# Performance work log

Measured on AMD Instinct MI355X. Metric: run time of the kernel, lower is better.

## Reference

```python
import jax, jax.numpy as jnp
import numpy as np

NHEAD = 8  # nn.MultiheadAttention default in TransformerDecoderLayerOptimal
LN_EPS = 1e-5


def layer_norm(x, g, b):
    m = x.mean(-1, keepdims=True)
    v = ((x - m) ** 2).mean(-1, keepdims=True)
    return (x - m) * jax.lax.rsqrt(v + LN_EPS) * g + b


def setup_inputs() -> dict:
    key = jax.random.key(0)
    ks = jax.random.split(key, 16)
    B, S, F0, D, L, C, DF = 32, 1024, 2048, 768, 100, 1000, 10
    sc = 0.02
    return {
        "x": jax.random.normal(ks[0], (B, S, F0), jnp.float32),
        "y": jax.random.normal(ks[1], (L, D), jnp.float32),
        "embed_W": jax.random.normal(ks[2], (D, F0), jnp.float32) * sc,
        "embed_b": jnp.zeros((D,), jnp.float32),
        "Wq": jax.random.normal(ks[3], (D, D), jnp.float32) * sc,
        "Wk": jax.random.normal(ks[4], (D, D), jnp.float32) * sc,
        "Wv": jax.random.normal(ks[5], (D, D), jnp.float32) * sc,
        "bq": jnp.zeros((D,), jnp.float32),
        "bk": jnp.zeros((D,), jnp.float32),
        "bv": jnp.zeros((D,), jnp.float32),
        "Wo": jax.random.normal(ks[6], (D, D), jnp.float32) * sc,
        "bo": jnp.zeros((D,), jnp.float32),
        "ln1_g": jnp.ones((D,), jnp.float32), "ln1_b": jnp.zeros((D,), jnp.float32),
        "ln2_g": jnp.ones((D,), jnp.float32), "ln2_b": jnp.zeros((D,), jnp.float32),
        "ln3_g": jnp.ones((D,), jnp.float32), "ln3_b": jnp.zeros((D,), jnp.float32),
        "ffn_W1": jax.random.normal(ks[7], (D, D), jnp.float32) * sc,  # dim_feedforward = d_model
        "ffn_b1": jnp.zeros((D,), jnp.float32),
        "ffn_W2": jax.random.normal(ks[8], (D, D), jnp.float32) * sc,
        "ffn_b2": jnp.zeros((D,), jnp.float32),
        "dup_pool": jax.random.normal(ks[9], (L, 2 * D, DF), jnp.float32) * sc,
        "dup_bias": jnp.zeros((C,), jnp.float32),
    }


def reference(x, y, embed_W, embed_b, Wq, Wk, Wv, bq, bk, bv, Wo, bo,
              ln1_g, ln1_b, ln2_g, ln2_b, ln3_g, ln3_b,
              ffn_W1, ffn_b1, ffn_W2, ffn_b2, dup_pool, dup_bias):
    B = x.shape[0]
    L, D = y.shape
    H, hd = NHEAD, D // NHEAD
    num_classes = dup_bias.shape[0]

    # embed_standart + relu : (B,S,F0) -> (B,S,D)
    mem = jax.nn.relu(jnp.einsum('bsf,df->bsd', x, embed_W) + embed_b)

    # tgt = query_embed repeated over batch (batch-first here)
    tgt0 = jnp.broadcast_to(y[None], (B, L, D))

    # TransformerDecoderLayerOptimal (eval mode: dropout = identity)
    t = layer_norm(tgt0 + tgt0, ln1_g, ln1_b)  # tgt + dropout1(tgt)

    # cross multi-head attention
    q = (jnp.einsum('bld,ed->ble', t, Wq) + bq).reshape(B, L, H, hd)
    k = (jnp.einsum('bsd,ed->bse', mem, Wk) + bk).reshape(B, -1, H, hd)
    v = (jnp.einsum('bsd,ed->bse', mem, Wv) + bv).reshape(B, -1, H, hd)
    scores = jnp.einsum('blhe,bshe->bhls', q, k) / np.float32(np.sqrt(hd))
    attn = jax.nn.softmax(scores, axis=-1)           # (B,H,L,S)
    ao = jnp.einsum('bhls,bshe->blhe', attn, v).reshape(B, L, D)
    ao = jnp.einsum('bld,ed->ble', ao, Wo) + bo
    t = layer_norm(t + ao, ln2_g, ln2_b)

    # FFN
    f = jnp.einsum('bld,ed->ble',
                   jax.nn.relu(jnp.einsum('bld,ed->ble', t, ffn_W1) + ffn_b1),
                   ffn_W2) + ffn_b2
    h = layer_norm(t + f, ln3_g, ln3_b)              # (B,L,D)

    # concat label embedding after h, then GroupFC (per-label grouped matmul)
    hcat = jnp.concatenate([h, tgt0], axis=-1)       # (B,L,2D)
    out_extrap = jnp.einsum('bld,ldf->blf', hcat, dup_pool)  # (B,L,DF)
    logits = out_extrap.reshape(B, -1)[:, :num_classes] + dup_bias

    a_score = attn.mean(axis=1)                      # MHA averages heads: (B,L,S)
    return logits, a_score
```

## Files before the change

### kernel.cpp

```cpp
#include <hip/hip_runtime.h>

typedef unsigned short u16;
typedef __bf16 bf16x8 __attribute__((ext_vector_type(8)));
typedef short s16x8 __attribute__((ext_vector_type(8)));
typedef u16 u16x4 __attribute__((ext_vector_type(4)));
typedef float f32x4 __attribute__((ext_vector_type(4)));

__device__ __forceinline__ float b2f(u16 u) {
  union { unsigned u32; float f; } x; x.u32 = ((unsigned)u) << 16; return x.f;
}
__device__ __forceinline__ u16 f2b(float f) {
  union { float f; unsigned u; } x; x.f = f;
  unsigned r = x.u + 0x7fffu + ((x.u >> 16) & 1u);
  return (u16)(r >> 16);
}

template <int F32>
__device__ __forceinline__ s16x8 load8(const void* __restrict__ p, size_t idx) {
  if (F32) {
    const float* f = (const float*)p + idx;
    f32x4 a = *(const f32x4*)f;
    f32x4 b = *(const f32x4*)(f + 4);
    s16x8 r;
    r[0] = (short)f2b(a[0]); r[1] = (short)f2b(a[1]);
    r[2] = (short)f2b(a[2]); r[3] = (short)f2b(a[3]);
    r[4] = (short)f2b(b[0]); r[5] = (short)f2b(b[1]);
    r[6] = (short)f2b(b[2]); r[7] = (short)f2b(b[3]);
    return r;
  } else {
    return *(const s16x8*)((const u16*)p + idx);
  }
}

template <int RELU, int AF32, int BF32, int TRANSC = 0>
__global__ __launch_bounds__(256) void gemm_bt_kernel(
    const void* __restrict__ A, const void* __restrict__ Bt,
    const float* __restrict__ bias, u16* __restrict__ C,
    int M, int N, int K) {
  __shared__ u16 As[128][32];
  __shared__ u16 Bs[128][32];
  const int tid = threadIdx.x;
  const int lane = tid & 63;
  const int wave = tid >> 6;
  const int wm = wave >> 1, wn = wave & 1;
  const int lr = tid >> 2;
  const int lk = (tid & 3) << 3;
  const int tn = blockIdx.x, tm = blockIdx.y;
  const size_t abase = (size_t)tm * 128 * K;
  const size_t bbase = (size_t)tn * 128 * K;
  const int fr = lane & 15;
  const int fk = (lane >> 4) << 3;
  f32x4 acc[4][4] = {};

  for (int k0 = 0; k0 < K; k0 += 32) {
    *(s16x8*)&As[lr][lk]      = load8<AF32>(A, abase + (size_t)lr * K + k0 + lk);
    *(s16x8*)&As[lr + 64][lk] = load8<AF32>(A, abase + (size_t)(lr + 64) * K + k0 + lk);
    *(s16x8*)&Bs[lr][lk]      = load8<BF32>(Bt, bbase + (size_t)lr * K + k0 + lk);
    *(s16x8*)&Bs[lr + 64][lk] = load8<BF32>(Bt, bbase + (size_t)(lr + 64) * K + k0 + lk);
    __syncthreads();
    bf16x8 af[4], bfv[4];
#pragma unroll
    for (int i = 0; i < 4; ++i)
      af[i] = __builtin_bit_cast(bf16x8, *(const s16x8*)&As[wm * 64 + i * 16 + fr][fk]);
#pragma unroll
    for (int j = 0; j < 4; ++j)
      bfv[j] = __builtin_bit_cast(bf16x8, *(const s16x8*)&Bs[wn * 64 + j * 16 + fr][fk]);
#pragma unroll
    for (int i = 0; i < 4; ++i)
#pragma unroll
      for (int j = 0; j < 4; ++j)
        acc[i][j] = __builtin_amdgcn_mfma_f32_16x16x32_bf16(af[i], bfv[j], acc[i][j], 0, 0, 0);
    __syncthreads();
  }

  const int row0 = tm * 128 + wm * 64 + ((lane >> 4) << 2);
  const int col0 = tn * 128 + wn * 64 + fr;
  if (TRANSC) {
#pragma unroll
    for (int j = 0; j < 4; ++j) {
      const int col = col0 + j * 16;
      const float bv = bias[col];
#pragma unroll
      for (int i = 0; i < 4; ++i) {
        const int row = row0 + i * 16;
        u16x4 pk;
#pragma unroll
        for (int r = 0; r < 4; ++r) {
          float v = acc[i][j][r] + bv;
          if (RELU) v = fmaxf(v, 0.f);
          pk[r] = f2b(v);
        }
        size_t idx = ((size_t)(row >> 10) * N + col) * 1024 + (row & 1023);
        *(u16x4*)&C[idx] = pk;
      }
    }
  } else {
#pragma unroll
    for (int j = 0; j < 4; ++j) {
      const int col = col0 + j * 16;
      const float bv = bias[col];
#pragma unroll
      for (int i = 0; i < 4; ++i) {
#pragma unroll
        for (int r = 0; r < 4; ++r) {
          float v = acc[i][j][r] + bv;
          if (RELU) v = fmaxf(v, 0.f);
          C[(size_t)(row0 + i * 16 + r) * N + col] = f2b(v);
        }
      }
    }
  }
}

__device__ __forceinline__ void block_stats(float s, float s2, float* red, int tid,
                                            float& S, float& S2) {
#pragma unroll
  for (int o = 32; o > 0; o >>= 1) { s += __shfl_xor(s, o); s2 += __shfl_xor(s2, o); }
  if ((tid & 63) == 0) { red[tid >> 6] = s; red[4 + (tid >> 6)] = s2; }
  __syncthreads();
  S = red[0] + red[1] + red[2] + red[3];
  S2 = red[4] + red[5] + red[6] + red[7];
}

__global__ __launch_bounds__(256) void t_kernel(const float* __restrict__ y,
                                                const float* __restrict__ g,
                                                const float* __restrict__ bb,
                                                float* __restrict__ t) {
  const int l = blockIdx.x, tid = threadIdx.x;
  __shared__ float red[8];
  float xv[3], s = 0.f, s2 = 0.f;
#pragma unroll
  for (int i = 0; i < 3; ++i) {
    int e = tid + i * 256;
    float v = 2.f * y[(size_t)l * 768 + e];
    xv[i] = v; s += v; s2 += v * v;
  }
  float S, S2;
  block_stats(s, s2, red, tid, S, S2);
  float mean = S * (1.f / 768.f);
  float var = S2 * (1.f / 768.f) - mean * mean;
  float inv = rsqrtf(var + 1e-5f);
#pragma unroll
  for (int i = 0; i < 3; ++i) {
    int e = tid + i * 256;
    t[(size_t)l * 768 + e] = (xv[i] - mean) * inv * g[e] + bb[e];
  }
}

__global__ __launch_bounds__(256) void q_kernel(const float* __restrict__ t,
                                                const float* __restrict__ Wq,
                                                const float* __restrict__ bq,
                                                float* __restrict__ q) {
  const int l = blockIdx.x, tid = threadIdx.x;
  __shared__ __align__(16) float ts[768];
  for (int i = tid; i < 768; i += 256) ts[i] = t[(size_t)l * 768 + i];
  __syncthreads();
  for (int e = tid; e < 768; e += 256) {
    const float* wr = Wq + (size_t)e * 768;
    float acc = bq[e];
    for (int j = 0; j < 768; j += 4) {
      f32x4 wv = *(const f32x4*)&wr[j];
      f32x4 tv = *(const f32x4*)&ts[j];
      acc += wv[0] * tv[0] + wv[1] * tv[1] + wv[2] * tv[2] + wv[3] * tv[3];
    }
    q[(size_t)l * 768 + e] = acc;
  }
}

__global__ __launch_bounds__(256) void c2_kernel(const float* __restrict__ y,
                                                 const float* __restrict__ pool,
                                                 const float* __restrict__ dbias,
                                                 float* __restrict__ c2) {
  const int l = blockIdx.x, tid = threadIdx.x, lane = tid & 63, w = tid >> 6;
  for (int j = w; j < 10; j += 4) {
    float acc = 0.f;
    for (int d = lane; d < 768; d += 64)
      acc += y[(size_t)l * 768 + d] * pool[((size_t)l * 1536 + 768 + d) * 10 + j];
#pragma unroll
    for (int o = 32; o > 0; o >>= 1) acc += __shfl_xor(acc, o);
    if (lane == 0) c2[l * 10 + j] = acc + dbias[l * 10 + j];
  }
}

__global__ __launch_bounds__(512) void attn_kernel(
    const float* __restrict__ q,
    const u16* __restrict__ kmat,
    const u16* __restrict__ vt,
    u16* __restrict__ ao,
    float* __restrict__ ascore) {
  const int b = blockIdx.x;
  const int l0 = blockIdx.y * 13;
  __shared__ float sc[13][1028];
  __shared__ __align__(16) u16 qs[16][96];
  __shared__ float rinv[16];
  const int tid = threadIdx.x;
  const int lane = tid & 63;
  const int w = tid >> 6;
  const int fr = lane & 15;
  const int hi = lane >> 4;
  const int fk = hi << 3;
  const int sfr = (fr < 13) ? fr : 12;
  float areg[26];
#pragma unroll
  for (int j = 0; j < 26; ++j) areg[j] = 0.f;

  for (int h = 0; h < 8; ++h) {
    for (int i = tid; i < 192; i += 512) {
      int r = i / 12, c8 = (i % 12) * 8;
      int l = l0 + r;
      s16x8 v = {};
      if (r < 13 && l < 100) v = load8<1>(q, (size_t)l * 768 + h * 96 + c8);
      *(s16x8*)&qs[r][c8] = v;
    }
    __syncthreads();
    bf16x8 af[3];
#pragma unroll
    for (int kk = 0; kk < 3; ++kk)
      af[kk] = __builtin_bit_cast(bf16x8, *(const s16x8*)&qs[fr][kk * 32 + fk]);
    const u16* kbase = kmat + (size_t)(b * 1024 + w * 128 + fr) * 768 + h * 96 + fk;
#pragma unroll 2
    for (int nt = 0; nt < 8; ++nt) {
      f32x4 acc = {};
      const u16* kp = kbase + (size_t)nt * 16 * 768;
#pragma unroll
      for (int kk = 0; kk < 3; ++kk) {
        bf16x8 bf = __builtin_bit_cast(bf16x8, *(const s16x8*)(kp + kk * 32));
        acc = __builtin_amdgcn_mfma_f32_16x16x32_bf16(af[kk], bf, acc, 0, 0, 0);
      }
      const int s = w * 128 + nt * 16 + fr;
#pragma unroll
      for (int r = 0; r < 4; ++r) {
        int lr = hi * 4 + r;
        if (lr < 13) sc[lr][s] = acc[r] * 0.10206207261596575f;
      }
    }
    __syncthreads();
    for (int r = w; r < 13; r += 8) {
      float m = -1e30f;
      for (int i = lane; i < 1024; i += 64) m = fmaxf(m, sc[r][i]);
#pragma unroll
      for (int o = 32; o > 0; o >>= 1) m = fmaxf(m, __shfl_xor(m, o));
      float sum = 0.f;
      for (int i = lane; i < 1024; i += 64) {
        float e = __expf(sc[r][i] - m);
        sc[r][i] = e; sum += e;
      }
#pragma unroll
      for (int o = 32; o > 0; o >>= 1) sum += __shfl_xor(sum, o);
      if (lane == 0) rinv[r] = 1.f / sum;
    }
    __syncthreads();
#pragma unroll
    for (int j = 0; j < 26; ++j) {
      int i = tid + j * 512;
      int r = i >> 10;
      areg[j] += sc[r][i & 1023] * rinv[r];
    }
    f32x4 pacc[6];
#pragma unroll
    for (int nt = 0; nt < 6; ++nt) pacc[nt] = (f32x4){0.f, 0.f, 0.f, 0.f};
    const u16* vbase = vt + (size_t)(b * 768 + h * 96 + fr) * 1024 + w * 128 + fk;
#pragma unroll 2
    for (int ks = 0; ks < 4; ++ks) {
      const float* sp = &sc[sfr][w * 128 + ks * 32 + fk];
      bf16x8 paf;
#pragma unroll
      for (int j2 = 0; j2 < 8; ++j2) paf[j2] = (__bf16)sp[j2];
#pragma unroll
      for (int nt = 0; nt < 6; ++nt) {
        bf16x8 vf = __builtin_bit_cast(bf16x8,
            *(const s16x8*)(vbase + (size_t)nt * 16 * 1024 + ks * 32));
        pacc[nt] = __builtin_amdgcn_mfma_f32_16x16x32_bf16(paf, vf, pacc[nt], 0, 0, 0);
      }
    }
    __syncthreads();
    float* red = &sc[0][0];
#pragma unroll
    for (int nt = 0; nt < 6; ++nt) {
#pragma unroll
      for (int r = 0; r < 4; ++r) {
        int lr = hi * 4 + r;
        if (lr < 13) red[(w * 13 + lr) * 96 + nt * 16 + fr] = pacc[nt][r];
      }
    }
    __syncthreads();
    for (int i = tid; i < 1248; i += 512) {
      int lr = i / 96, d = i % 96;
      float s = 0.f;
#pragma unroll
      for (int w8 = 0; w8 < 8; ++w8) s += red[(w8 * 13 + lr) * 96 + d];
      int l = l0 + lr;
      if (l < 100) ao[(size_t)(b * 100 + l) * 768 + h * 96 + d] = f2b(s * rinv[lr]);
    }
    __syncthreads();
  }
#pragma unroll
  for (int j = 0; j < 26; ++j) {
    int i = tid + j * 512;
    int r = i >> 10;
    int l = l0 + r;
    if (l < 100) ascore[(size_t)(b * 100 + l) * 1024 + (i & 1023)] = areg[j] * 0.125f;
  }
}

__global__ __launch_bounds__(256) void ln_kernel(
    const float* __restrict__ base, const u16* __restrict__ add,
    const float* __restrict__ g, const float* __restrict__ bb,
    float* __restrict__ outf, u16* __restrict__ outb, int base_per_l) {
  const int row = blockIdx.x, tid = threadIdx.x;
  __shared__ float red[8];
  const size_t boff = (size_t)(base_per_l ? (row % 100) : row) * 768;
  const size_t aoff = (size_t)row * 768;
  float xv[3], s = 0.f, s2 = 0.f;
#pragma unroll
  for (int i = 0; i < 3; ++i) {
    int e = tid + i * 256;
    float v = base[boff + e] + b2f(add[aoff + e]);
    xv[i] = v; s += v; s2 += v * v;
  }
  float S, S2;
  block_stats(s, s2, red, tid, S, S2);
  float mean = S * (1.f / 768.f);
  float var = S2 * (1.f / 768.f) - mean * mean;
  float inv = rsqrtf(var + 1e-5f);
#pragma unroll
  for (int i = 0; i < 3; ++i) {
    int e = tid + i * 256;
    float o = (xv[i] - mean) * inv * g[e] + bb[e];
    if (outf) outf[aoff + e] = o;
    if (outb) outb[aoff + e] = f2b(o);
  }
}

__global__ __launch_bounds__(256) void groupfc_kernel(
    const u16* __restrict__ h, const float* __restrict__ pool,
    const float* __restrict__ c2, float* __restrict__ logits) {
  const int l = blockIdx.x, tid = threadIdx.x;
  __shared__ float ps[768][10];
  for (int i = tid; i < 7680; i += 256) ps[i / 10][i % 10] = pool[(size_t)l * 15360 + i];
  __syncthreads();
  for (int idx = tid; idx < 320; idx += 256) {
    int bb = idx / 10, j = idx % 10;
    const u16* hr = h + (size_t)(bb * 100 + l) * 768;
    float acc = c2[l * 10 + j];
    for (int d0 = 0; d0 < 768; d0 += 8) {
      s16x8 hv = *(const s16x8*)&hr[d0];
#pragma unroll
      for (int e = 0; e < 8; ++e) acc += b2f((u16)hv[e]) * ps[d0 + e][j];
    }
    logits[bb * 1000 + l * 10 + j] = acc;
  }
}

extern "C" void kernel_launch(void* const* d_in, const int* in_sizes, int n_in,
                              void* d_out, int out_size, void* d_ws, size_t ws_size,
                              hipStream_t stream) {
  (void)in_sizes; (void)n_in; (void)out_size; (void)ws_size;
  const float* x      = (const float*)d_in[0];
  const float* y      = (const float*)d_in[1];
  const float* embedW = (const float*)d_in[2];
  const float* embedb = (const float*)d_in[3];
  const float* Wq     = (const float*)d_in[4];
  const float* Wk     = (const float*)d_in[5];
  const float* Wv     = (const float*)d_in[6];
  const float* bq     = (const float*)d_in[7];
  const float* bk     = (const float*)d_in[8];
  const float* bv     = (const float*)d_in[9];
  const float* Wo     = (const float*)d_in[10];
  const float* bo     = (const float*)d_in[11];
  const float* ln1g   = (const float*)d_in[12];
  const float* ln1b   = (const float*)d_in[13];
  const float* ln2g   = (const float*)d_in[14];
  const float* ln2b   = (const float*)d_in[15];
  const float* ln3g   = (const float*)d_in[16];
  const float* ln3b   = (const float*)d_in[17];
  const float* W1     = (const float*)d_in[18];
  const float* b1     = (const float*)d_in[19];
  const float* W2     = (const float*)d_in[20];
  const float* b2     = (const float*)d_in[21];
  const float* pool   = (const float*)d_in[22];
  const float* dbias  = (const float*)d_in[23];

  char* w = (char*)d_ws;
  u16* kws = (u16*)(w);
  u16* vt  = (u16*)(w + 50331648);
  char* R  = w + 100663296;
  u16*   mem = (u16*)R;
  u16*   ao  = (u16*)(R + 0);
  u16*   u1  = (u16*)(R + 4915200);
  u16*   t2b = (u16*)(R + 9830400);
  u16*   f1  = (u16*)(R + 14745600);
  u16*   f2  = (u16*)(R + 19660800);
  u16*   hb  = (u16*)(R + 24576000);
  float* t2f = (float*)(R + 29491200);
  float* tf  = (float*)(w + 150994944);
  float* qf  = (float*)(w + 150994944 + 307200);
  float* c2  = (float*)(w + 150994944 + 614400);

  float* logits = (float*)d_out;
  float* ascore = (float*)d_out + 32000;

  t_kernel<<<dim3(100), dim3(256), 0, stream>>>(y, ln1g, ln1b, tf);
  q_kernel<<<dim3(100), dim3(256), 0, stream>>>(tf, Wq, bq, qf);
  c2_kernel<<<dim3(100), dim3(256), 0, stream>>>(y, pool, dbias, c2);

  gemm_bt_kernel<1, 1, 1><<<dim3(6, 256), dim3(256), 0, stream>>>(x, embedW, embedb, mem, 32768, 768, 2048);
  gemm_bt_kernel<0, 0, 1><<<dim3(6, 256), dim3(256), 0, stream>>>(mem, Wk, bk, kws, 32768, 768, 768);
  gemm_bt_kernel<0, 0, 1, 1><<<dim3(6, 256), dim3(256), 0, stream>>>(mem, Wv, bv, vt, 32768, 768, 768);

  attn_kernel<<<dim3(32, 8), dim3(512), 0, stream>>>(qf, kws, vt, ao, ascore);

  gemm_bt_kernel<0, 0, 1><<<dim3(6, 25), dim3(256), 0, stream>>>(ao, Wo, bo, u1, 3200, 768, 768);
  ln_kernel<<<dim3(3200), dim3(256), 0, stream>>>(tf, u1, ln2g, ln2b, t2f, t2b, 1);
  gemm_bt_kernel<1, 0, 1><<<dim3(6, 25), dim3(256), 0, stream>>>(t2b, W1, b1, f1, 3200, 768, 768);
  gemm_bt_kernel<0, 0, 1><<<dim3(6, 25), dim3(256), 0, stream>>>(f1, W2, b2, f2, 3200, 768, 768);
  ln_kernel<<<dim3(3200), dim3(256), 0, stream>>>(t2f, f2, ln3g, ln3b, (float*)nullptr, hb, 0);
  groupfc_kernel<<<dim3(100), dim3(256), 0, stream>>>(hb, pool, c2, logits);
}
```

Baseline: 1.112 ms.

## Pre-convert weights to bf16, use direct global-to-LDS loads, XCD-aware tile remap

Weights are converted to bf16 by small conversion kernels each call, so the GEMMs no longer convert fp32 B tiles inside the K loop. Tiles that are already bf16 are loaded with global_load_lds, which writes straight into shared memory without passing through registers. The grid becomes 1D, with a block-to-tile remap that gives each XCD a contiguous range of tiles to improve L2 locality. The conversion kernels add extra launches and traffic, and the scratch regions they write into are reused across stages, so buffer aliasing has to stay correct.

```diff
diff --git a/kernel.cpp b/kernel.cpp
--- a/kernel.cpp
+++ b/kernel.cpp
@@ -32,9 +32,31 @@
   }
 }
 
-template <int RELU, int AF32, int BF32, int TRANSC = 0>
+__device__ __forceinline__ void gl16(const u16* g, u16* l) {
+  __builtin_amdgcn_global_load_lds(
+      (const __attribute__((address_space(1))) void*)g,
+      (__attribute__((address_space(3))) void*)l, 16, 0, 0);
+}
+
+__global__ __launch_bounds__(256) void cvt_kernel(const float* __restrict__ in,
+                                                  u16* __restrict__ out, int n8) {
+  int i = blockIdx.x * 256 + threadIdx.x;
+  if (i < n8) *(s16x8*)&out[(size_t)i * 8] = load8<1>(in, (size_t)i * 8);
+}
+
+__global__ __launch_bounds__(256) void cvt3_kernel(
+    const float* __restrict__ a, const float* __restrict__ b,
+    const float* __restrict__ c, u16* __restrict__ oa, u16* __restrict__ ob,
+    u16* __restrict__ oc, int n8) {
+  int i = blockIdx.x * 256 + threadIdx.x;
+  const float* in = blockIdx.y == 0 ? a : (blockIdx.y == 1 ? b : c);
+  u16* out = blockIdx.y == 0 ? oa : (blockIdx.y == 1 ? ob : oc);
+  if (i < n8) *(s16x8*)&out[(size_t)i * 8] = load8<1>(in, (size_t)i * 8);
+}
+
+template <int RELU, int AF32, int TRANSC>
 __global__ __launch_bounds__(256) void gemm_bt_kernel(
-    const void* __restrict__ A, const void* __restrict__ Bt,
+    const void* __restrict__ A, const u16* __restrict__ Bt,
     const float* __restrict__ bias, u16* __restrict__ C,
     int M, int N, int K) {
   __shared__ u16 As[128][32];
@@ -43,20 +65,43 @@
   const int lane = tid & 63;
   const int wave = tid >> 6;
   const int wm = wave >> 1, wn = wave & 1;
-  const int lr = tid >> 2;
-  const int lk = (tid & 3) << 3;
-  const int tn = blockIdx.x, tm = blockIdx.y;
+  const int nwg = gridDim.x;
+  const int orig = blockIdx.x;
+  const int q = nwg >> 3, r = nwg & 7;
+  const int xcd = orig & 7, loc = orig >> 3;
+  const int wgid = (xcd < r ? xcd * (q + 1) : r * (q + 1) + (xcd - r) * q) + loc;
+  const int NT = N >> 7;
+  const int tn = wgid % NT, tm = wgid / NT;
   const size_t abase = (size_t)tm * 128 * K;
   const size_t bbase = (size_t)tn * 128 * K;
   const int fr = lane & 15;
   const int fk = (lane >> 4) << 3;
+  const int grow = lane >> 2;
+  const int gkoff = (lane & 3) << 3;
+  const u16* bgp = Bt + bbase + (size_t)(wave * 32 + grow) * K + gkoff;
+  u16* lB0 = &Bs[wave * 32][0];
+  u16* lB1 = &Bs[wave * 32 + 16][0];
+  const u16* agp = nullptr;
+  u16 *lA0 = nullptr, *lA1 = nullptr;
+  if (!AF32) {
+    agp = (const u16*)A + abase + (size_t)(wave * 32 + grow) * K + gkoff;
+    lA0 = &As[wave * 32][0];
+    lA1 = &As[wave * 32 + 16][0];
+  }
+  const int lr = tid >> 2;
+  const int lk = (tid & 3) << 3;
   f32x4 acc[4][4] = {};
 
   for (int k0 = 0; k0 < K; k0 += 32) {
-    *(s16x8*)&As[lr][lk]      = load8<AF32>(A, abase + (size_t)lr * K + k0 + lk);
-    *(s16x8*)&As[lr + 64][lk] = load8<AF32>(A, abase + (size_t)(lr + 64) * K + k0 + lk);
-    *(s16x8*)&Bs[lr][lk]      = load8<BF32>(Bt, bbase + (size_t)lr * K + k0 + lk);
-    *(s16x8*)&Bs[lr + 64][lk] = load8<BF32>(Bt, bbase + (size_t)(lr + 64) * K + k0 + lk);
+    if (AF32) {
+      *(s16x8*)&As[lr][lk]      = load8<1>(A, abase + (size_t)lr * K + k0 + lk);
+      *(s16x8*)&As[lr + 64][lk] = load8<1>(A, abase + (size_t)(lr + 64) * K + k0 + lk);
+    } else {
+      gl16(agp + k0, lA0);
+      gl16(agp + k0 + (size_t)16 * K, lA1);
+    }
+    gl16(bgp + k0, lB0);
+    gl16(bgp + k0 + (size_t)16 * K, lB1);
     __syncthreads();
     bf16x8 af[4], bfv[4];
 #pragma unroll
@@ -85,10 +130,10 @@
         const int row = row0 + i * 16;
         u16x4 pk;
 #pragma unroll
-        for (int r = 0; r < 4; ++r) {
-          float v = acc[i][j][r] + bv;
+        for (int r2 = 0; r2 < 4; ++r2) {
+          float v = acc[i][j][r2] + bv;
           if (RELU) v = fmaxf(v, 0.f);
-          pk[r] = f2b(v);
+          pk[r2] = f2b(v);
         }
         size_t idx = ((size_t)(row >> 10) * N + col) * 1024 + (row & 1023);
         *(u16x4*)&C[idx] = pk;
@@ -102,10 +147,10 @@
 #pragma unroll
       for (int i = 0; i < 4; ++i) {
 #pragma unroll
-        for (int r = 0; r < 4; ++r) {
-          float v = acc[i][j][r] + bv;
+        for (int r2 = 0; r2 < 4; ++r2) {
+          float v = acc[i][j][r2] + bv;
           if (RELU) v = fmaxf(v, 0.f);
-          C[(size_t)(row0 + i * 16 + r) * N + col] = f2b(v);
+          C[(size_t)(row0 + i * 16 + r2) * N + col] = f2b(v);
         }
       }
     }
@@ -230,8 +275,8 @@
       const int s = w * 128 + nt * 16 + fr;
 #pragma unroll
       for (int r = 0; r < 4; ++r) {
-        int lr = hi * 4 + r;
-        if (lr < 13) sc[lr][s] = acc[r] * 0.10206207261596575f;
+        int lr2 = hi * 4 + r;
+        if (lr2 < 13) sc[lr2][s] = acc[r] * 0.10206207261596575f;
       }
     }
     __syncthreads();
@@ -279,18 +324,18 @@
     for (int nt = 0; nt < 6; ++nt) {
 #pragma unroll
       for (int r = 0; r < 4; ++r) {
-        int lr = hi * 4 + r;
-        if (lr < 13) red[(w * 13 + lr) * 96 + nt * 16 + fr] = pacc[nt][r];
+        int lr2 = hi * 4 + r;
+        if (lr2 < 13) red[(w * 13 + lr2) * 96 + nt * 16 + fr] = pacc[nt][r];
       }
     }
     __syncthreads();
     for (int i = tid; i < 1248; i += 512) {
-      int lr = i / 96, d = i % 96;
+      int lr2 = i / 96, d = i % 96;
       float s = 0.f;
 #pragma unroll
-      for (int w8 = 0; w8 < 8; ++w8) s += red[(w8 * 13 + lr) * 96 + d];
-      int l = l0 + lr;
-      if (l < 100) ao[(size_t)(b * 100 + l) * 768 + h * 96 + d] = f2b(s * rinv[lr]);
+      for (int w8 = 0; w8 < 8; ++w8) s += red[(w8 * 13 + lr2) * 96 + d];
+      int l = l0 + lr2;
+      if (l < 100) ao[(size_t)(b * 100 + l) * 768 + h * 96 + d] = f2b(s * rinv[lr2]);
     }
     __syncthreads();
   }
@@ -396,24 +441,34 @@
   float* tf  = (float*)(w + 150994944);
   float* qf  = (float*)(w + 150994944 + 307200);
   float* c2  = (float*)(w + 150994944 + 614400);
+  u16* wbE = (u16*)(w + 50331648);
+  u16* wbK = (u16*)(w + 50331648 + 3145728);
+  u16* wbV = (u16*)(w + 150994944 + 1048576);
+  u16* wbO = (u16*)(w + 0);
+  u16* wb1 = (u16*)(w + 1179648);
+  u16* wb2 = (u16*)(w + 2359296);
 
   float* logits = (float*)d_out;
   float* ascore = (float*)d_out + 32000;
 
+  cvt_kernel<<<dim3(768), dim3(256), 0, stream>>>(embedW, wbE, 196608);
+  cvt_kernel<<<dim3(288), dim3(256), 0, stream>>>(Wk, wbK, 73728);
+  cvt_kernel<<<dim3(288), dim3(256), 0, stream>>>(Wv, wbV, 73728);
   t_kernel<<<dim3(100), dim3(256), 0, stream>>>(y, ln1g, ln1b, tf);
   q_kernel<<<dim3(100), dim3(256), 0, stream>>>(tf, Wq, bq, qf);
   c2_kernel<<<dim3(100), dim3(256), 0, stream>>>(y, pool, dbias, c2);
 
-  gemm_bt_kernel<1, 1, 1><<<dim3(6, 256), dim3(256), 0, stream>>>(x, embedW, embedb, mem, 32768, 768, 2048);
-  gemm_bt_kernel<0, 0, 1><<<dim3(6, 256), dim3(256), 0, stream>>>(mem, Wk, bk, kws, 32768, 768, 768);
-  gemm_bt_kernel<0, 0, 1, 1><<<dim3(6, 256), dim3(256), 0, stream>>>(mem, Wv, bv, vt, 32768, 768, 768);
+  gemm_bt_kernel<1, 1, 0><<<dim3(1536), dim3(256), 0, stream>>>(x, wbE, embedb, mem, 32768, 768, 2048);
+  gemm_bt_kernel<0, 0, 0><<<dim3(1536), dim3(256), 0, stream>>>(mem, wbK, bk, kws, 32768, 768, 768);
+  gemm_bt_kernel<0, 0, 1><<<dim3(1536), dim3(256), 0, stream>>>(mem, wbV, bv, vt, 32768, 768, 768);
 
   attn_kernel<<<dim3(32, 8), dim3(512), 0, stream>>>(qf, kws, vt, ao, ascore);
 
-  gemm_bt_kernel<0, 0, 1><<<dim3(6, 25), dim3(256), 0, stream>>>(ao, Wo, bo, u1, 3200, 768, 768);
+  cvt3_kernel<<<dim3(288, 3), dim3(256), 0, stream>>>(Wo, W1, W2, wbO, wb1, wb2, 73728);
+  gemm_bt_kernel<0, 0, 0><<<dim3(150), dim3(256), 0, stream>>>(ao, wbO, bo, u1, 3200, 768, 768);
   ln_kernel<<<dim3(3200), dim3(256), 0, stream>>>(tf, u1, ln2g, ln2b, t2f, t2b, 1);
-  gemm_bt_kernel<1, 0, 1><<<dim3(6, 25), dim3(256), 0, stream>>>(t2b, W1, b1, f1, 3200, 768, 768);
-  gemm_bt_kernel<0, 0, 1><<<dim3(6, 25), dim3(256), 0, stream>>>(f1, W2, b2, f2, 3200, 768, 768);
+  gemm_bt_kernel<1, 0, 0><<<dim3(150), dim3(256), 0, stream>>>(t2b, wb1, b1, f1, 3200, 768, 768);
+  gemm_bt_kernel<0, 0, 0><<<dim3(150), dim3(256), 0, stream>>>(f1, wb2, b2, f2, 3200, 768, 768);
   ln_kernel<<<dim3(3200), dim3(256), 0, stream>>>(t2f, f2, ln3g, ln3b, (float*)nullptr, hb, 0);
   groupfc_kernel<<<dim3(100), dim3(256), 0, stream>>>(hb, pool, c2, logits);
 }
```

After: 1.010 ms. 9.2% less time.
